# Kernel tuning notes

Measured on AMD Instinct MI355X. Metric: run time of the kernel, lower is better.

Reference implementation:

```python
import jax, jax.numpy as jnp
import numpy as np

B, T, C = 2, 2048, 1024
NUM_HEADS, QK_LEN, V_LEN = 16, 64, 64


def setup_inputs() -> dict:
    key = jax.random.key(0)
    ks = jax.random.split(key, 11)
    s = 0.02
    return {
        "Q": jax.random.normal(ks[0], (B, T, C), jnp.float32),
        "K": jax.random.normal(ks[1], (B, T, C), jnp.float32),
        "V": jax.random.normal(ks[2], (B, T, C), jnp.float32),
        # Linear weights stored as (in, out); y = x @ W + b
        "Wq": jax.random.normal(ks[3], (C, NUM_HEADS * QK_LEN), jnp.float32) * s,
        "bq": jnp.zeros((NUM_HEADS * QK_LEN,), jnp.float32),
        "Wk": jax.random.normal(ks[4], (C, NUM_HEADS * QK_LEN), jnp.float32) * s,
        "bk": jnp.zeros((NUM_HEADS * QK_LEN,), jnp.float32),
        "Wv": jax.random.normal(ks[5], (C, NUM_HEADS * V_LEN), jnp.float32) * s,
        "bv": jnp.zeros((NUM_HEADS * V_LEN,), jnp.float32),
        "Wo": jax.random.normal(ks[6], (NUM_HEADS * V_LEN, C), jnp.float32) * s,
        "bo": jnp.zeros((C,), jnp.float32),
    }


def _split_heads(x, n_heads, d):
    b, t, _ = x.shape
    return x.reshape(b, t, n_heads, d).transpose(0, 2, 1, 3)  # (B,H,T,d)


def reference(Q, K, V, Wq, bq, Wk, bk, Wv, bv, Wo, bo):
    q = _split_heads(Q @ Wq + bq, NUM_HEADS, QK_LEN)   # (B,H,T,dk)
    k = _split_heads(K @ Wk + bk, NUM_HEADS, QK_LEN)   # (B,H,T,dk)
    v = _split_heads(V @ Wv + bv, NUM_HEADS, V_LEN)    # (B,H,T,dv)

    scale = 1.0 / jnp.sqrt(jnp.asarray(QK_LEN, q.dtype))
    scores = jnp.einsum("bhqd,bhkd->bhqk", q, k) * scale  # (B,H,T,T)
    attn = jax.nn.softmax(scores, axis=-1)
    out = jnp.einsum("bhqk,bhkd->bhqd", attn, v)           # (B,H,T,dv)

    out = out.transpose(0, 2, 1, 3).reshape(Q.shape[0], Q.shape[1], NUM_HEADS * V_LEN)
    return out @ Wo + bo
```

## Files before the change

### kernel.cpp

```cpp
#include <hip/hip_runtime.h>
#include <hip/hip_bf16.h>
#include <math.h>

constexpr int B = 2, T = 2048, C = 1024, H = 16, D = 64;
constexpr int M = B * T;
constexpr float SCALE_L2E = 0.125f * 1.4426950408889634f;

typedef __attribute__((ext_vector_type(8))) short s16x8;
typedef __attribute__((ext_vector_type(4))) short s16x4;
typedef __attribute__((ext_vector_type(4))) float fv4;

typedef unsigned short ushort_t;

static __device__ __forceinline__ ushort_t f2bf(float x) {
    union { float f; unsigned u; } c; c.f = x;
    unsigned u = c.u + 0x7FFFu + ((c.u >> 16) & 1u);
    return (ushort_t)(u >> 16);
}

#define GLDS(gp, lp) __builtin_amdgcn_global_load_lds( \
    (const __attribute__((address_space(1))) void*)(gp), \
    (__attribute__((address_space(3))) void*)(lp), 16, 0, 0)

__global__ __launch_bounds__(256) void convert_qkv(
    const float* __restrict__ Q, const float* __restrict__ K,
    const float* __restrict__ V, ushort_t* __restrict__ dst)
{
    size_t e = ((size_t)blockIdx.x * 256 + threadIdx.x) * 8;
    const float* src;
    size_t base;
    if (e < (size_t)M * C)          { src = Q; base = 0; }
    else if (e < 2 * (size_t)M * C) { src = K; base = (size_t)M * C; }
    else                            { src = V; base = 2 * (size_t)M * C; }
    const float* p = src + (e - base);
    float4 a = *(const float4*)p;
    float4 b = *(const float4*)(p + 4);
    union { s16x8 v; ushort_t u[8]; } o;
    o.u[0] = f2bf(a.x); o.u[1] = f2bf(a.y); o.u[2] = f2bf(a.z); o.u[3] = f2bf(a.w);
    o.u[4] = f2bf(b.x); o.u[5] = f2bf(b.y); o.u[6] = f2bf(b.z); o.u[7] = f2bf(b.w);
    *(s16x8*)(dst + e) = o.v;
}

__global__ __launch_bounds__(256) void transpose_w(
    const float* __restrict__ W0, const float* __restrict__ W1,
    const float* __restrict__ W2, const float* __restrict__ W3,
    ushort_t* __restrict__ Wt)
{
    const int s = blockIdx.z;
    const float* W = (s == 0) ? W0 : (s == 1) ? W1 : (s == 2) ? W2 : W3;
    const int k0 = blockIdx.x * 64, n0 = blockIdx.y * 64;
    __shared__ ushort_t tile[64][72];
    const int tid = threadIdx.x;
#pragma unroll
    for (int it = 0; it < 4; it++) {
        int f = it * 256 + tid;
        int r = f >> 4, c4 = (f & 15) * 4;
        float4 x = *(const float4*)(W + (size_t)(k0 + r) * C + n0 + c4);
        tile[r][c4 + 0] = f2bf(x.x);
        tile[r][c4 + 1] = f2bf(x.y);
        tile[r][c4 + 2] = f2bf(x.z);
        tile[r][c4 + 3] = f2bf(x.w);
    }
    __syncthreads();
#pragma unroll
    for (int it = 0; it < 4; it++) {
        int f = it * 256 + tid;
        int rr = f >> 4, c4 = (f & 15) * 4;
        union { s16x4 v; ushort_t u[4]; } u;
#pragma unroll
        for (int j = 0; j < 4; j++) u.u[j] = tile[c4 + j][rr];
        *(s16x4*)(Wt + (size_t)(s * 1024 + n0 + rr) * 1024 + k0 + c4) = u.v;
    }
}

__global__ __launch_bounds__(256) void transpose_v(
    const ushort_t* __restrict__ vw, ushort_t* __restrict__ vt)
{
    __shared__ ushort_t tile[64][72];
    const int tid = threadIdx.x;
    const int t0 = blockIdx.x * 64;
    const int bh = blockIdx.y;
    const ushort_t* src = vw + ((size_t)bh * T + t0) * D;
#pragma unroll
    for (int it = 0; it < 2; it++) {
        int f = it * 256 + tid;
        int row = f >> 3, c8 = (f & 7) * 8;
        *(s16x8*)&tile[row][c8] = *(const s16x8*)(src + (size_t)row * D + c8);
    }
    __syncthreads();
    ushort_t* dst = vt + (size_t)bh * D * T + t0;
#pragma unroll
    for (int it = 0; it < 4; it++) {
        int f = it * 256 + tid;
        int d = f >> 4, t4 = (f & 15) * 4;
        union { s16x4 v; ushort_t u[4]; } u;
#pragma unroll
        for (int j = 0; j < 4; j++) u.u[j] = tile[t4 + j][d];
        *(s16x4*)(dst + (size_t)d * T + t4) = u.v;
    }
}

__global__ __launch_bounds__(256) void gemm_qkv(
    const ushort_t* __restrict__ qkv, const ushort_t* __restrict__ Wt,
    const float* __restrict__ bq, const float* __restrict__ bk,
    const float* __restrict__ bv,
    ushort_t* __restrict__ qw, ushort_t* __restrict__ kw,
    ushort_t* __restrict__ vw)
{
    __shared__ ushort_t As[2][128 * 32];
    __shared__ ushort_t Bs[2][128 * 32];

    const int tid = threadIdx.x;
    const int w = tid >> 6, lane = tid & 63;
    const int quad = lane >> 4, lc = lane & 15;
    const int wm = w & 1, wn = w >> 1;

    const int nt = blockIdx.x;
    const int m0 = blockIdx.y * 128;
    const int s = nt >> 3;
    const int nsec0 = (nt & 7) * 128;

    const ushort_t* Abase = qkv + (size_t)s * M * C;
    const ushort_t* Btbase = Wt + (size_t)nt * 128 * 1024;

    const int srow = (w << 4) + (lane >> 2);
    const int ske  = (lane & 3) * 8;

    fv4 acc[4][4] = {};

    auto stage = [&](int k0, int buf) {
#pragma unroll
        for (int i = 0; i < 2; i++) {
            int row = i * 64 + srow;
            GLDS(Abase + (size_t)(m0 + row) * 1024 + k0 + ske,
                 As[buf] + i * 2048 + w * 512);
            GLDS(Btbase + (size_t)row * 1024 + k0 + ske,
                 Bs[buf] + i * 2048 + w * 512);
        }
    };

    stage(0, 0);
    __syncthreads();

    for (int k0 = 0; k0 < 1024; k0 += 32) {
        const int cur = (k0 >> 5) & 1;
        if (k0 + 32 < 1024) stage(k0 + 32, cur ^ 1);

        s16x8 af[4], bf[4];
#pragma unroll
        for (int ms = 0; ms < 4; ms++)
            af[ms] = *(const s16x8*)(As[cur] + (wm * 64 + ms * 16 + lc) * 32 + quad * 8);
#pragma unroll
        for (int ns = 0; ns < 4; ns++)
            bf[ns] = *(const s16x8*)(Bs[cur] + (wn * 64 + ns * 16 + lc) * 32 + quad * 8);
#pragma unroll
        for (int ms = 0; ms < 4; ms++)
#pragma unroll
            for (int ns = 0; ns < 4; ns++)
                acc[ms][ns] = __builtin_amdgcn_mfma_f32_16x16x32_bf16(
                    af[ms], bf[ns], acc[ms][ns], 0, 0, 0);
        __syncthreads();
    }

    const float* biasp = (s == 0) ? bq : (s == 1) ? bk : bv;
    const float premul = (s == 0) ? SCALE_L2E : 1.0f;
    ushort_t* outp = (s == 0) ? qw : (s == 1) ? kw : vw;

#pragma unroll
    for (int ns = 0; ns < 4; ns++) {
        const int nl = nsec0 + wn * 64 + ns * 16 + lc;
        const float bias = biasp[nl];
        const int h_ = nl >> 6, d_ = nl & 63;
#pragma unroll
        for (int ms = 0; ms < 4; ms++) {
#pragma unroll
            for (int r = 0; r < 4; r++) {
                int m = m0 + wm * 64 + ms * 16 + quad * 4 + r;
                float val = (acc[ms][ns][r] + bias) * premul;
                int b_ = m >> 11, t_ = m & (T - 1);
                size_t bh = (size_t)(b_ * H + h_);
                outp[((bh * T + t_) << 6) + d_] = f2bf(val);
            }
        }
    }
}

__global__ __launch_bounds__(256) void gemm_final(
    const ushort_t* __restrict__ A, const ushort_t* __restrict__ Wot,
    const float* __restrict__ bo, float* __restrict__ out)
{
    __shared__ ushort_t As[2][128 * 32];
    __shared__ ushort_t Bs[2][64 * 32];

    const int tid = threadIdx.x;
    const int w = tid >> 6, lane = tid & 63;
    const int quad = lane >> 4, lc = lane & 15;
    const int wm = w & 1, wn = w >> 1;

    const int n0 = blockIdx.x * 64;
    const int m0 = blockIdx.y * 128;

    const int srow = (w << 4) + (lane >> 2);
    const int ske  = (lane & 3) * 8;

    fv4 acc[4][2] = {};

    auto stage = [&](int k0, int buf) {
        GLDS(A + (size_t)(m0 + srow) * 1024 + k0 + ske,      As[buf] + w * 512);
        GLDS(A + (size_t)(m0 + 64 + srow) * 1024 + k0 + ske, As[buf] + 2048 + w * 512);
        GLDS(Wot + (size_t)(n0 + srow) * 1024 + k0 + ske,    Bs[buf] + w * 512);
    };

    stage(0, 0);
    __syncthreads();

    for (int k0 = 0; k0 < 1024; k0 += 32) {
        const int cur = (k0 >> 5) & 1;
        if (k0 + 32 < 1024) stage(k0 + 32, cur ^ 1);

        s16x8 af[4], bf[2];
#pragma unroll
        for (int ms = 0; ms < 4; ms++)
            af[ms] = *(const s16x8*)(As[cur] + (wm * 64 + ms * 16 + lc) * 32 + quad * 8);
#pragma unroll
        for (int ns = 0; ns < 2; ns++)
            bf[ns] = *(const s16x8*)(Bs[cur] + (wn * 32 + ns * 16 + lc) * 32 + quad * 8);
#pragma unroll
        for (int ms = 0; ms < 4; ms++)
#pragma unroll
            for (int ns = 0; ns < 2; ns++)
                acc[ms][ns] = __builtin_amdgcn_mfma_f32_16x16x32_bf16(
                    af[ms], bf[ns], acc[ms][ns], 0, 0, 0);
        __syncthreads();
    }

#pragma unroll
    for (int ns = 0; ns < 2; ns++) {
        const int n = n0 + wn * 32 + ns * 16 + lc;
        const float bias = bo[n];
#pragma unroll
        for (int ms = 0; ms < 4; ms++) {
#pragma unroll
            for (int r = 0; r < 4; r++) {
                int m = m0 + wm * 64 + ms * 16 + quad * 4 + r;
                out[(size_t)m * 1024 + n] = acc[ms][ns][r] + bias;
            }
        }
    }
}

__global__ __launch_bounds__(256) void attn(
    const ushort_t* __restrict__ q, const ushort_t* __restrict__ k,
    const ushort_t* __restrict__ vT, ushort_t* __restrict__ o)
{
    __shared__ ushort_t ks[2][64 * 64];
    __shared__ ushort_t vs[2][64 * 64];
    __shared__ ushort_t ps[4][32][72];

    const int tid = threadIdx.x;
    const int w = tid >> 6, lane = tid & 63;
    const int quad = lane >> 4, lc = lane & 15;
    const int cs = lc & 7;
    const int qt = blockIdx.x;
    const int bh = blockIdx.y;

    s16x8 aq[2][2];
    const ushort_t* qb = q + ((size_t)bh * T + qt * 128 + w * 32) * D;
#pragma unroll
    for (int j = 0; j < 2; j++)
#pragma unroll
        for (int h = 0; h < 2; h++)
            aq[j][h] = *(const s16x8*)(qb + (size_t)(j * 16 + lc) * D + h * 32 + quad * 8);

    fv4 accO[2][4] = {};
    float psum[2] = {0.f, 0.f};

    const ushort_t* kb0 = k + (size_t)bh * T * D;
    const ushort_t* vb0 = vT + (size_t)bh * D * T;

    const int sr8 = lane >> 3;
    const int sch = (lane & 7) ^ sr8;

    auto stage = [&](int kt, int buf) {
#pragma unroll
        for (int i = 0; i < 2; i++) {
            const int r = w * 16 + i * 8 + sr8;
            GLDS(kb0 + (size_t)(kt * 64 + r) * 64 + sch * 8,
                 ks[buf] + (w * 16 + i * 8) * 64);
            GLDS(vb0 + (size_t)r * T + kt * 64 + sch * 8,
                 vs[buf] + (w * 16 + i * 8) * 64);
        }
    };

    stage(0, 0);
    __syncthreads();

    for (int kt = 0; kt < T / 64; kt++) {
        const int cur = kt & 1;
        if (kt + 1 < T / 64) stage(kt + 1, cur ^ 1);

        fv4 accST[2][4] = {};
#pragma unroll
        for (int t4 = 0; t4 < 4; t4++) {
            const int row = t4 * 16 + lc;
            s16x8 ak0 = *(const s16x8*)(ks[cur] + row * 64 + ((quad ^ cs) << 3));
            s16x8 ak1 = *(const s16x8*)(ks[cur] + row * 64 + (((quad + 4) ^ cs) << 3));
#pragma unroll
            for (int j = 0; j < 2; j++) {
                accST[j][t4] = __builtin_amdgcn_mfma_f32_16x16x32_bf16(
                    ak0, aq[j][0], accST[j][t4], 0, 0, 0);
                accST[j][t4] = __builtin_amdgcn_mfma_f32_16x16x32_bf16(
                    ak1, aq[j][1], accST[j][t4], 0, 0, 0);
            }
        }

#pragma unroll
        for (int j = 0; j < 2; j++) {
#pragma unroll
            for (int t4 = 0; t4 < 4; t4++) {
                union { s16x4 v; ushort_t u[4]; } pk;
#pragma unroll
                for (int r = 0; r < 4; r++) {
                    float p = __builtin_amdgcn_exp2f(accST[j][t4][r]);
                    pk.u[r] = f2bf(p);
                    psum[j] += p;
                }
                *(s16x4*)&ps[w][j * 16 + lc][t4 * 16 + quad * 4] = pk.v;
            }
        }

        s16x8 pb[2][2];
#pragma unroll
        for (int j = 0; j < 2; j++)
#pragma unroll
            for (int g = 0; g < 2; g++)
                pb[j][g] = *(const s16x8*)&ps[w][j * 16 + lc][g * 32 + quad * 8];

#pragma unroll
        for (int t4 = 0; t4 < 4; t4++) {
            const int row = t4 * 16 + lc;
#pragma unroll
            for (int g = 0; g < 2; g++) {
                s16x8 av = *(const s16x8*)(vs[cur] + row * 64 + (((g * 4 + quad) ^ cs) << 3));
#pragma unroll
                for (int j = 0; j < 2; j++)
                    accO[j][t4] = __builtin_amdgcn_mfma_f32_16x16x32_bf16(
                        av, pb[j][g], accO[j][t4], 0, 0, 0);
            }
        }

        __syncthreads();
    }

#pragma unroll
    for (int j = 0; j < 2; j++) {
        psum[j] += __shfl_xor(psum[j], 16);
        psum[j] += __shfl_xor(psum[j], 32);
    }

    const int b_ = bh >> 4, h_ = bh & 15;
#pragma unroll
    for (int j = 0; j < 2; j++) {
        float inv = 1.0f / psum[j];
        int row = qt * 128 + w * 32 + j * 16 + lc;
        ushort_t* op = o + ((size_t)b_ * T + row) * C + h_ * 64;
#pragma unroll
        for (int t4 = 0; t4 < 4; t4++) {
            union { s16x4 v; ushort_t u[4]; } u;
#pragma unroll
            for (int r = 0; r < 4; r++) u.u[r] = f2bf(accO[j][t4][r] * inv);
            *(s16x4*)(op + t4 * 16 + quad * 4) = u.v;
        }
    }
}

extern "C" void kernel_launch(void* const* d_in, const int* in_sizes, int n_in,
                              void* d_out, int out_size, void* d_ws, size_t ws_size,
                              hipStream_t stream)
{
    const float* Q  = (const float*)d_in[0];
    const float* K  = (const float*)d_in[1];
    const float* V  = (const float*)d_in[2];
    const float* Wq = (const float*)d_in[3];
    const float* bq = (const float*)d_in[4];
    const float* Wk = (const float*)d_in[5];
    const float* bk = (const float*)d_in[6];
    const float* Wv = (const float*)d_in[7];
    const float* bv = (const float*)d_in[8];
    const float* Wo = (const float*)d_in[9];
    const float* bo = (const float*)d_in[10];
    float* out = (float*)d_out;

    ushort_t* qkvbf = (ushort_t*)d_ws;
    ushort_t* Wt = qkvbf + (size_t)3 * M * C;
    ushort_t* qw = Wt + (size_t)4096 * 1024;
    ushort_t* kw = qw + (size_t)M * C;
    ushort_t* vw = kw + (size_t)M * C;
    ushort_t* vt = vw + (size_t)M * C;
    ushort_t* ow = qkvbf;
    ushort_t* Wot = Wt + (size_t)3072 * 1024;

    dim3 blk(256);
    convert_qkv<<<dim3(3 * M * C / 2048), blk, 0, stream>>>(Q, K, V, qkvbf);
    transpose_w<<<dim3(16, 16, 4), blk, 0, stream>>>(Wq, Wk, Wv, Wo, Wt);
    gemm_qkv<<<dim3(24, 32), blk, 0, stream>>>(qkvbf, Wt, bq, bk, bv, qw, kw, vw);
    transpose_v<<<dim3(T / 64, B * H), blk, 0, stream>>>(vw, vt);
    attn<<<dim3(T / 128, B * H), blk, 0, stream>>>(qw, kw, vt, ow);
    gemm_final<<<dim3(16, 32), blk, 0, stream>>>(ow, Wot, bo, out);
}
```

Before: 245.5 us.

## Split attention key tiles across warps and reduce partial outputs in LDS

The attention kernel now gives each block 64 query rows instead of 128. Its four warps form a 2x2 grid over query and key halves, and each warp processes 32 keys per tile, with partial O and row sums reduced through shared memory at the end. This doubles the grid to 1024 blocks for better occupancy and adds launch_bounds(256,4) with a smaller P buffer. The cost is that K/V tiles are staged twice as often per query row, plus extra syncs and an LDS reduction in the epilogue.

After: 241.9 us. No clear change (-1.5%).

```diff
diff --git a/kernel.cpp b/kernel.cpp
--- a/kernel.cpp
+++ b/kernel.cpp
@@ -249,23 +249,24 @@
     }
 }
 
-__global__ __launch_bounds__(256) void attn(
+__global__ __launch_bounds__(256, 4) void attn(
     const ushort_t* __restrict__ q, const ushort_t* __restrict__ k,
     const ushort_t* __restrict__ vT, ushort_t* __restrict__ o)
 {
-    __shared__ ushort_t ks[2][64 * 64];
-    __shared__ ushort_t vs[2][64 * 64];
-    __shared__ ushort_t ps[4][32][72];
+    __shared__ alignas(16) ushort_t ks[2][64 * 64];
+    __shared__ alignas(16) ushort_t vs[2][64 * 64];
+    __shared__ alignas(16) ushort_t ps[4 * 16 * 40];
 
     const int tid = threadIdx.x;
     const int w = tid >> 6, lane = tid & 63;
     const int quad = lane >> 4, lc = lane & 15;
     const int cs = lc & 7;
+    const int qsub = w & 1, ksub = w >> 1;
     const int qt = blockIdx.x;
     const int bh = blockIdx.y;
 
     s16x8 aq[2][2];
-    const ushort_t* qb = q + ((size_t)bh * T + qt * 128 + w * 32) * D;
+    const ushort_t* qb = q + ((size_t)bh * T + qt * 64 + qsub * 32) * D;
 #pragma unroll
     for (int j = 0; j < 2; j++)
 #pragma unroll
@@ -295,58 +296,57 @@
     stage(0, 0);
     __syncthreads();
 
+    ushort_t* psw = ps + (w * 16) * 40;
+
     for (int kt = 0; kt < T / 64; kt++) {
         const int cur = kt & 1;
         if (kt + 1 < T / 64) stage(kt + 1, cur ^ 1);
 
-        fv4 accST[2][4] = {};
-#pragma unroll
-        for (int t4 = 0; t4 < 4; t4++) {
-            const int row = t4 * 16 + lc;
+        fv4 accST[2][2] = {};
+#pragma unroll
+        for (int t4k = 0; t4k < 2; t4k++) {
+            const int row = ksub * 32 + t4k * 16 + lc;
             s16x8 ak0 = *(const s16x8*)(ks[cur] + row * 64 + ((quad ^ cs) << 3));
             s16x8 ak1 = *(const s16x8*)(ks[cur] + row * 64 + (((quad + 4) ^ cs) << 3));
 #pragma unroll
             for (int j = 0; j < 2; j++) {
-                accST[j][t4] = __builtin_amdgcn_mfma_f32_16x16x32_bf16(
-                    ak0, aq[j][0], accST[j][t4], 0, 0, 0);
-                accST[j][t4] = __builtin_amdgcn_mfma_f32_16x16x32_bf16(
-                    ak1, aq[j][1], accST[j][t4], 0, 0, 0);
+                accST[j][t4k] = __builtin_amdgcn_mfma_f32_16x16x32_bf16(
+                    ak0, aq[j][0], accST[j][t4k], 0, 0, 0);
+                accST[j][t4k] = __builtin_amdgcn_mfma_f32_16x16x32_bf16(
+                    ak1, aq[j][1], accST[j][t4k], 0, 0, 0);
             }
         }
 
+        s16x8 av[4];
+#pragma unroll
+        for (int t4v = 0; t4v < 4; t4v++) {
+            const int row = t4v * 16 + lc;
+            av[t4v] = *(const s16x8*)(vs[cur] + row * 64 + (((ksub * 4 + quad) ^ cs) << 3));
+        }
+
 #pragma unroll
         for (int j = 0; j < 2; j++) {
-#pragma unroll
-            for (int t4 = 0; t4 < 4; t4++) {
+            float c0 = 0.f, c1 = 0.f;
+#pragma unroll
+            for (int t4k = 0; t4k < 2; t4k++) {
                 union { s16x4 v; ushort_t u[4]; } pk;
-#pragma unroll
-                for (int r = 0; r < 4; r++) {
-                    float p = __builtin_amdgcn_exp2f(accST[j][t4][r]);
-                    pk.u[r] = f2bf(p);
-                    psum[j] += p;
-                }
-                *(s16x4*)&ps[w][j * 16 + lc][t4 * 16 + quad * 4] = pk.v;
+                float p0 = __builtin_amdgcn_exp2f(accST[j][t4k][0]);
+                float p1 = __builtin_amdgcn_exp2f(accST[j][t4k][1]);
+                float p2 = __builtin_amdgcn_exp2f(accST[j][t4k][2]);
+                float p3 = __builtin_amdgcn_exp2f(accST[j][t4k][3]);
+                pk.u[0] = f2bf(p0); pk.u[1] = f2bf(p1);
+                pk.u[2] = f2bf(p2); pk.u[3] = f2bf(p3);
+                if (t4k == 0) c0 = (p0 + p1) + (p2 + p3);
+                else          c1 = (p0 + p1) + (p2 + p3);
+                *(s16x4*)(psw + lc * 40 + t4k * 16 + quad * 4) = pk.v;
             }
-        }
-
-        s16x8 pb[2][2];
-#pragma unroll
-        for (int j = 0; j < 2; j++)
-#pragma unroll
-            for (int g = 0; g < 2; g++)
-                pb[j][g] = *(const s16x8*)&ps[w][j * 16 + lc][g * 32 + quad * 8];
-
-#pragma unroll
-        for (int t4 = 0; t4 < 4; t4++) {
-            const int row = t4 * 16 + lc;
-#pragma unroll
-            for (int g = 0; g < 2; g++) {
-                s16x8 av = *(const s16x8*)(vs[cur] + row * 64 + (((g * 4 + quad) ^ cs) << 3));
-#pragma unroll
-                for (int j = 0; j < 2; j++)
-                    accO[j][t4] = __builtin_amdgcn_mfma_f32_16x16x32_bf16(
-                        av, pb[j][g], accO[j][t4], 0, 0, 0);
-            }
+            psum[j] += c0 + c1;
+
+            s16x8 pb = *(const s16x8*)(psw + lc * 40 + quad * 8);
+#pragma unroll
+            for (int t4v = 0; t4v < 4; t4v++)
+                accO[j][t4v] = __builtin_amdgcn_mfma_f32_16x16x32_bf16(
+                    av[t4v], pb, accO[j][t4v], 0, 0, 0);
         }
 
         __syncthreads();
@@ -358,18 +358,44 @@
         psum[j] += __shfl_xor(psum[j], 32);
     }
 
-    const int b_ = bh >> 4, h_ = bh & 15;
-#pragma unroll
-    for (int j = 0; j < 2; j++) {
-        float inv = 1.0f / psum[j];
-        int row = qt * 128 + w * 32 + j * 16 + lc;
-        ushort_t* op = o + ((size_t)b_ * T + row) * C + h_ * 64;
-#pragma unroll
-        for (int t4 = 0; t4 < 4; t4++) {
-            union { s16x4 v; ushort_t u[4]; } u;
-#pragma unroll
-            for (int r = 0; r < 4; r++) u.u[r] = f2bf(accO[j][t4][r] * inv);
-            *(s16x4*)(op + t4 * 16 + quad * 4) = u.v;
+    float* sc = (float*)ps;
+#pragma unroll
+    for (int c = 0; c < 4; c++) {
+        const int j = c >> 1, tv = (c & 1) * 2;
+        __syncthreads();
+        if (ksub == 1) {
+            *(fv4*)(sc + ((qsub * 64 + lane) * 8))     = accO[j][tv];
+            *(fv4*)(sc + ((qsub * 64 + lane) * 8 + 4)) = accO[j][tv + 1];
+        }
+        __syncthreads();
+        if (ksub == 0) {
+            accO[j][tv]     += *(fv4*)(sc + ((qsub * 64 + lane) * 8));
+            accO[j][tv + 1] += *(fv4*)(sc + ((qsub * 64 + lane) * 8 + 4));
+        }
+    }
+    __syncthreads();
+    if (ksub == 1) {
+        sc[(qsub * 64 + lane) * 2]     = psum[0];
+        sc[(qsub * 64 + lane) * 2 + 1] = psum[1];
+    }
+    __syncthreads();
+    if (ksub == 0) {
+        psum[0] += sc[(qsub * 64 + lane) * 2];
+        psum[1] += sc[(qsub * 64 + lane) * 2 + 1];
+
+        const int b_ = bh >> 4, h_ = bh & 15;
+#pragma unroll
+        for (int j = 0; j < 2; j++) {
+            float inv = 1.0f / psum[j];
+            int row = qt * 64 + qsub * 32 + j * 16 + lc;
+            ushort_t* op = o + ((size_t)b_ * T + row) * C + h_ * 64;
+#pragma unroll
+            for (int t4v = 0; t4v < 4; t4v++) {
+                union { s16x4 v; ushort_t u[4]; } u;
+#pragma unroll
+                for (int r = 0; r < 4; r++) u.u[r] = f2bf(accO[j][t4v][r] * inv);
+                *(s16x4*)(op + t4v * 16 + quad * 4) = u.v;
+            }
         }
     }
 }
@@ -405,6 +431,6 @@
     transpose_w<<<dim3(16, 16, 4), blk, 0, stream>>>(Wq, Wk, Wv, Wo, Wt);
     gemm_qkv<<<dim3(24, 32), blk, 0, stream>>>(qkvbf, Wt, bq, bk, bv, qw, kw, vw);
     transpose_v<<<dim3(T / 64, B * H), blk, 0, stream>>>(vw, vt);
-    attn<<<dim3(T / 128, B * H), blk, 0, stream>>>(qw, kw, vt, ow);
+    attn<<<dim3(T / 64, B * H), blk, 0, stream>>>(qw, kw, vt, ow);
     gemm_final<<<dim3(16, 32), blk, 0, stream>>>(ow, Wot, bo, out);
 }
```
